# Kernel optimization log

Hardware: AMD Instinct MI355X
Metric: run time of the kernel (lower is better)

Reference implementation:

```python
import jax, jax.numpy as jnp
import numpy as np

N_NODES = 5000
N_STRUCT = 50
PER = N_NODES // N_STRUCT
K = 24
N_EDGES = N_NODES * K
MAX_EDGES = 32
D = 128
HEADS = 4
L = 2
M = 1
NSP = 4
ALL_SPECIES = np.array([1, 6, 7, 8])
R_CUT, R_TRANS = 5.0, 3.0
SPECIES_TABLE = jnp.full((9,), -1, dtype=jnp.int32).at[jnp.asarray(ALL_SPECIES)].set(jnp.arange(NSP, dtype=jnp.int32))

def _ln(x, w, b):
    m = jnp.mean(x, axis=-1, keepdims=True)
    v = jnp.var(x, axis=-1, keepdims=True)
    return (x - m) * jax.lax.rsqrt(v + 1e-5) * w + b

def _block(x, mask, Wq, Wk, Wv, Wo, l1w, l1b, l2w, l2b, W1, b1, W2, b2):
    n, t, d = x.shape
    dh = d // HEADS
    h = _ln(x, l1w, l1b)
    q = (h @ Wq).reshape(n, t, HEADS, dh)
    k = (h @ Wk).reshape(n, t, HEADS, dh)
    v = (h @ Wv).reshape(n, t, HEADS, dh)
    scores = jnp.einsum('nthd,nshd->nhts', q, k) * (1.0 / np.sqrt(dh))
    p = jax.nn.softmax(scores, axis=-1) * mask[:, None, None, :]  # cutoff-weighted keys
    x = x + jnp.einsum('nhts,nshd->nthd', p, v).reshape(n, t, d) @ Wo
    h2 = _ln(x, l2w, l2b)
    return x + jax.nn.gelu(h2 @ W1 + b1) @ W2 + b2

def _transformer(x, mask, params):
    for i in range(L):
        x = _block(x, mask, *(a[i] for a in params))
    return x

def _graph_indices(centers, neighbors):
    e_ids = jnp.arange(N_EDGES, dtype=jnp.int32)
    counts = jnp.zeros((N_NODES,), jnp.int32).at[centers].add(1)
    start = jnp.cumsum(counts) - counts
    slot = e_ids - start[centers]  # centers sorted by construction
    nef_idx = jnp.zeros((N_NODES, MAX_EDGES), jnp.int32).at[centers, slot].set(e_ids)
    nef_mask = jnp.arange(MAX_EDGES, dtype=jnp.int32)[None, :] < counts[:, None]
    keys = centers * N_NODES + neighbors
    order = jnp.argsort(keys)
    corr = order[jnp.searchsorted(keys[order], neighbors * N_NODES + centers)]
    return nef_idx, slot, nef_mask, corr

def _cutoff(r):
    x = (r - R_TRANS) / (R_CUT - R_TRANS)
    smooth = 0.5 * (1.0 + jnp.cos(jnp.pi * x))
    return jnp.where(r < R_TRANS, 1.0, jnp.where(r >= R_CUT, 0.0, smooth))

def _forward(positions, cells, cell_shifts, enc_Wcart, enc_emb_center, enc_emb_neigh, enc_Wcomp, t_Wq, t_Wk, t_Wv, t_Wo, t_ln1w, t_ln1b, t_ln2w, t_ln2b, t_W1, t_b1, t_W2, t_b2, g_contr, g_Wq, g_Wk, g_Wv, g_Wo, g_ln1w, g_ln1b, g_ln2w, g_ln2b, g_W1, g_b1, g_W2, g_b2, readout_W, composition_weights, numbers, centers, neighbors):
    seg = jnp.repeat(jnp.arange(N_STRUCT, dtype=jnp.int32), PER)  # sorted structure ids
    ev = positions[neighbors] - positions[centers] + jnp.einsum('ia,iab->ib', cell_shifts, cells[seg[centers]])
    radial = _cutoff(jnp.sqrt(jnp.sum(ev * ev, axis=-1)))
    elem = SPECIES_TABLE[numbers]
    nef_idx, slot, nef_mask, corr = _graph_indices(centers, neighbors)
    radial_nef = jnp.where(nef_mask, radial[nef_idx], 0.0)
    feats = jnp.concatenate([ev[nef_idx] @ enc_Wcart, enc_emb_center[elem[centers][nef_idx]], enc_emb_neigh[elem[neighbors][nef_idx]]], axis=-1) @ enc_Wcomp
    tparams = (t_Wq, t_Wk, t_Wv, t_Wo, t_ln1w, t_ln1b, t_ln2w, t_ln2b, t_W1, t_b1, t_W2, t_b2)
    feats = _transformer(feats, radial_nef, tparams)
    gparams = (g_Wq, g_Wk, g_Wv, g_Wo, g_ln1w, g_ln1b, g_ln2w, g_ln2b, g_W1, g_b1, g_W2, g_b2)
    for m in range(M):
        new = feats[centers, slot]  # nef -> edge list
        new = jnp.concatenate([new, new[corr]], axis=-1) @ g_contr[m]
        new = _transformer(new[nef_idx], radial_nef, tuple(a[m] for a in gparams))
        feats = feats + new
    ee = (feats @ readout_W)[..., 0] * radial_nef  # [N, MAX_EDGES]
    struct_e = jax.ops.segment_sum(jnp.sum(ee, axis=1), seg, num_segments=N_STRUCT, indices_are_sorted=True)
    comp = jax.ops.segment_sum(jax.nn.one_hot(elem, NSP, dtype=jnp.float32), seg, num_segments=N_STRUCT, indices_are_sorted=True)
    return struct_e + comp @ composition_weights

def setup_inputs():
    key = jax.random.key(0)
    ks = jax.random.split(key, 24)
    deltas = np.concatenate([np.arange(1, K // 2 + 1), -np.arange(1, K // 2 + 1)])
    nb_local = (np.arange(PER)[:, None] + deltas[None, :]) % PER  # symmetric circulant graph per structure
    neighbors = (nb_local[None, :, :] + (np.arange(N_STRUCT) * PER)[:, None, None]).reshape(-1)
    centers = np.repeat(np.arange(N_NODES), K)
    def w(i, shape, s=0.05):
        return (jax.random.normal(ks[i], shape) * s).astype(jnp.float32)
    return {
        'positions': jax.random.normal(ks[0], (N_NODES, 3), dtype=jnp.float32) * 2.0,
        'cells': jnp.tile(jnp.eye(3, dtype=jnp.float32) * 20.0, (N_STRUCT, 1, 1)),
        'cell_shifts': jnp.zeros((N_EDGES, 3), dtype=jnp.float32),
        'enc_Wcart': w(2, (3, D), 0.5),
        'enc_emb_center': w(3, (NSP, D), 1.0),
        'enc_emb_neigh': w(4, (NSP, D), 1.0),
        'enc_Wcomp': w(5, (3 * D, D)),
        't_Wq': w(6, (L, D, D)), 't_Wk': w(7, (L, D, D)), 't_Wv': w(8, (L, D, D)), 't_Wo': w(9, (L, D, D)),
        't_ln1w': jnp.ones((L, D), jnp.float32), 't_ln1b': jnp.zeros((L, D), jnp.float32),
        't_ln2w': jnp.ones((L, D), jnp.float32), 't_ln2b': jnp.zeros((L, D), jnp.float32),
        't_W1': w(10, (L, D, 4 * D)), 't_b1': jnp.zeros((L, 4 * D), jnp.float32),
        't_W2': w(11, (L, 4 * D, D)), 't_b2': jnp.zeros((L, D), jnp.float32),
        'g_contr': w(12, (M, 2 * D, D)),
        'g_Wq': w(13, (M, L, D, D)), 'g_Wk': w(14, (M, L, D, D)), 'g_Wv': w(15, (M, L, D, D)), 'g_Wo': w(16, (M, L, D, D)),
        'g_ln1w': jnp.ones((M, L, D), jnp.float32), 'g_ln1b': jnp.zeros((M, L, D), jnp.float32),
        'g_ln2w': jnp.ones((M, L, D), jnp.float32), 'g_ln2b': jnp.zeros((M, L, D), jnp.float32),
        'g_W1': w(17, (M, L, D, 4 * D)), 'g_b1': jnp.zeros((M, L, 4 * D), jnp.float32),
        'g_W2': w(18, (M, L, 4 * D, D)), 'g_b2': jnp.zeros((M, L, D), jnp.float32),
        'readout_W': w(19, (D, 1)),
        'composition_weights': w(20, (NSP,), 1.0),
        'numbers': jnp.asarray(ALL_SPECIES, dtype=jnp.int32)[jax.random.randint(ks[1], (N_NODES,), 0, NSP)],
        'centers': jnp.asarray(centers, dtype=jnp.int32),
        'neighbors': jnp.asarray(neighbors, dtype=jnp.int32),
    }

def reference(positions, cells, cell_shifts, enc_Wcart, enc_emb_center, enc_emb_neigh, enc_Wcomp, t_Wq, t_Wk, t_Wv, t_Wo, t_ln1w, t_ln1b, t_ln2w, t_ln2b, t_W1, t_b1, t_W2, t_b2, g_contr, g_Wq, g_Wk, g_Wv, g_Wo, g_ln1w, g_ln1b, g_ln2w, g_ln2b, g_W1, g_b1, g_W2, g_b2, readout_W, composition_weights, numbers, centers, neighbors):
    return _forward(positions, cells, cell_shifts, enc_Wcart, enc_emb_center, enc_emb_neigh, enc_Wcomp, t_Wq, t_Wk, t_Wv, t_Wo, t_ln1w, t_ln1b, t_ln2w, t_ln2b, t_W1, t_b1, t_W2, t_b2, g_contr, g_Wq, g_Wk, g_Wv, g_Wo, g_ln1w, g_ln1b, g_ln2w, g_ln2b, g_W1, g_b1, g_W2, g_b2, readout_W, composition_weights, numbers, centers, neighbors)
```

## Files before the change

### kernel.cpp

```cpp
#include <hip/hip_runtime.h>
#include <hip/hip_bf16.h>
#include <math.h>

#define N_NODES 5000
#define N_STRUCT 50
#define PER 100
#define K_NB 24
#define N_EDGES (N_NODES*K_NB)
#define TMAX 32
#define D 128
#define FF 512
#define NTOK (N_NODES*TMAX)

typedef short bf16x8 __attribute__((ext_vector_type(8)));
typedef float f32x4  __attribute__((ext_vector_type(4)));
#define MFMA_B16(a,b,c) __builtin_amdgcn_mfma_f32_16x16x32_bf16(a,b,c,0,0,0)

__device__ __forceinline__ short f2bf(float x){
    return (short)((__float_as_uint(x) + 0x8000u) >> 16);
}
__device__ __forceinline__ short f2bf_rn(float x){
    unsigned u = __float_as_uint(x);
    return (short)((u + 0x7FFFu + ((u>>16)&1u)) >> 16);
}

__device__ __forceinline__ float gelu_f(float x){
    float arg = x * fmaf(x*x, -0.07135481627f, -1.5957691216057308f);
    return x * __builtin_amdgcn_rcpf(1.f + __expf(arg));
}

__device__ __forceinline__ float cutoff_f(float r){
    if (r < 3.f) return 1.f;
    if (r >= 5.f) return 0.f;
    float x = (r-3.f)*0.5f;
    return 0.5f*(1.f + cosf(3.14159265358979323846f * x));
}

__global__ void k_zero(float* out){
    for (int i = threadIdx.x; i < N_STRUCT; i += 64) out[i] = 0.f;
}

__global__ void k_elem(const int* __restrict__ numbers, int* __restrict__ ELEM){
    int i = blockIdx.x*256 + threadIdx.x;
    if (i < N_NODES){
        int z = numbers[i];
        ELEM[i] = (z==1)?0:(z==6)?1:(z==7)?2:(z==8)?3:-1;
    }
}

__global__ void k_prep(const float* __restrict__ Wcart, const float* __restrict__ embc,
                       const float* __restrict__ embn, const float* __restrict__ Wcomp,
                       float* __restrict__ W3, float* __restrict__ ECn, float* __restrict__ ENn){
    int j = threadIdx.x;
    for (int a = 0; a < 3; a++){
        float s = 0;
        for (int i = 0; i < 128; i++) s += Wcart[a*128+i]*Wcomp[i*128+j];
        W3[a*128+j] = s;
    }
    for (int sp = 0; sp < 4; sp++){
        float s1 = 0, s2 = 0;
        for (int i = 0; i < 128; i++){
            s1 += embc[sp*128+i]*Wcomp[(128+i)*128+j];
            s2 += embn[sp*128+i]*Wcomp[(256+i)*128+j];
        }
        ECn[sp*128+j] = s1; ENn[sp*128+j] = s2;
    }
}

__global__ void k_wt(const float* tWq, const float* tWk, const float* tWv, const float* tWo,
                     const float* tW1, const float* tW2, const float* gWq, const float* gWk,
                     const float* gWv, const float* gWo, const float* gW1, const float* gW2,
                     const float* gct, short* __restrict__ WT){
    const int  sel[25]  = {0,0,1,1,2,2,3,3,4,4,5,5,6,6,7,7,8,8,9,9,10,10,11,11,12};
    const int  lin[25]  = {7,7,7,7,7,7,7,7,7,7,9,9,7,7,7,7,7,7,7,7,7,7,9,9,8};
    const int  lout[25] = {7,7,7,7,7,7,7,7,9,9,7,7,7,7,7,7,7,7,7,7,9,9,7,7,7};
    const int  soff[25] = {0,16384,0,16384,0,16384,0,16384,0,65536,0,65536,
                           0,16384,0,16384,0,16384,0,16384,0,65536,0,65536,0};
    const int  doff[25] = {0,16384,32768,49152,65536,81920,98304,114688,
                           131072,196608,262144,327680,
                           393216,409600,425984,442368,458752,475136,491520,507904,
                           524288,589824,655360,720896,786432};
    int gid = blockIdx.x*256 + threadIdx.x;
    if (gid >= 819200) return;
    int r = 0, base = 0;
    while (true){
        int sz = 1 << (lin[r]+lout[r]);
        if (gid < base + sz) break;
        base += sz; r++;
    }
    int d = gid - base;
    int j = d >> lin[r], i = d & ((1<<lin[r])-1);
    const float* src;
    switch (sel[r]){
        case 0: src=tWq; break; case 1: src=tWk; break; case 2: src=tWv; break; case 3: src=tWo; break;
        case 4: src=tW1; break; case 5: src=tW2; break;
        case 6: src=gWq; break; case 7: src=gWk; break; case 8: src=gWv; break; case 9: src=gWo; break;
        case 10: src=gW1; break; case 11: src=gW2; break; default: src=gct; break;
    }
    float v = src[soff[r] + (i<<lout[r]) + j];
    if (sel[r] == 0 || sel[r] == 6) v *= 0.17677669529663689f;
    WT[doff[r] + d] = f2bf_rn(v);
}

__global__ void k_edge(const float* __restrict__ pos, const float* __restrict__ cells,
                       const float* __restrict__ shifts, const int* __restrict__ centers,
                       const int* __restrict__ neighbors, float* __restrict__ EV,
                       float* __restrict__ RAD, int* __restrict__ CORR){
    int e = blockIdx.x*256 + threadIdx.x;
    if (e >= N_EDGES) return;
    int c = centers[e], nb = neighbors[e];
    int st = c / PER;
    const float* cell = cells + st*9;
    float s0 = shifts[e*3+0], s1 = shifts[e*3+1], s2 = shifts[e*3+2];
    float ex = pos[nb*3+0]-pos[c*3+0] + s0*cell[0]+s1*cell[3]+s2*cell[6];
    float ey = pos[nb*3+1]-pos[c*3+1] + s0*cell[1]+s1*cell[4]+s2*cell[7];
    float ez = pos[nb*3+2]-pos[c*3+2] + s0*cell[2]+s1*cell[5]+s2*cell[8];
    EV[e*3+0] = ex; EV[e*3+1] = ey; EV[e*3+2] = ez;
    RAD[e] = cutoff_f(sqrtf(ex*ex+ey*ey+ez*ez));
    int base = nb*K_NB, corr = base;
    for (int k2 = 0; k2 < K_NB; k2++){
        if (neighbors[base+k2] == c){ corr = base+k2; break; }
    }
    CORR[e] = corr;
}

__global__ void k_encode(const float* __restrict__ EV, const float* __restrict__ RAD,
                         const int* __restrict__ centers, const int* __restrict__ neighbors,
                         const int* __restrict__ ELEM, const float* __restrict__ W3,
                         const float* __restrict__ ECn, const float* __restrict__ ENn,
                         float* __restrict__ X, float* __restrict__ RADN){
    int row = blockIdx.x;
    int j = threadIdx.x;
    int n = row >> 5, s = row & 31;
    int e = (s < K_NB) ? (n*K_NB + s) : 0;
    int ec = ELEM[centers[e]], en = ELEM[neighbors[e]];
    float ev0 = EV[e*3+0], ev1 = EV[e*3+1], ev2 = EV[e*3+2];
    float v = ev0*W3[j] + ev1*W3[128+j] + ev2*W3[256+j] + ECn[ec*128+j] + ENn[en*128+j];
    X[(size_t)row*D + j] = v;
    if (j == 0) RADN[row] = (s < K_NB) ? RAD[e] : 0.f;
}

__global__ __launch_bounds__(256, 2) void k_attn_p(float* __restrict__ X,
        const short* __restrict__ Wqt, const short* __restrict__ Wkt,
        const short* __restrict__ Wvt, const short* __restrict__ Wot,
        const float* __restrict__ lnw, const float* __restrict__ lnb,
        const float* __restrict__ radn){
    __shared__ float xs[32*132];
    __shared__ short hh[32*136];
    __shared__ short Qs[32*136];
    __shared__ short Ks[32*136];
    __shared__ short VT[128*40];
    __shared__ short Ps[4*32*40];
    __shared__ float radl[32];
    const int tid = threadIdx.x, lane = tid & 63, w = tid >> 6;
    const int quad = lane >> 4, l16 = lane & 15;

    bf16x8 wQ[8], wK[8], wV[8], wO[8];
    #pragma unroll
    for (int mt = 0; mt < 2; mt++)
        #pragma unroll
        for (int kk = 0; kk < 4; kk++){
            int ro = (w*32 + mt*16 + l16)*128 + kk*32 + quad*8;
            wQ[mt*4+kk] = *(const bf16x8*)&Wqt[ro];
            wK[mt*4+kk] = *(const bf16x8*)&Wkt[ro];
            wV[mt*4+kk] = *(const bf16x8*)&Wvt[ro];
            wO[mt*4+kk] = *(const bf16x8*)&Wot[ro];
        }

    for (int node = blockIdx.x; node < N_NODES; node += 1024){
        float* Xn = X + (size_t)node*32*128;
        {
            int row = tid >> 3, l8 = tid & 7;
            f32x4 v[4];
            #pragma unroll
            for (int c = 0; c < 4; c++){
                v[c] = *(const f32x4*)&Xn[row*128 + l8*16 + c*4];
                *(f32x4*)&xs[row*132 + l8*16 + c*4] = v[c];
            }
            float s = 0, ss = 0;
            #pragma unroll
            for (int c = 0; c < 4; c++){
                #pragma unroll
                for (int k = 0; k < 4; k++){ s += v[c][k]; ss += v[c][k]*v[c][k]; }
            }
            #pragma unroll
            for (int m = 1; m < 8; m <<= 1){ s += __shfl_xor(s, m); ss += __shfl_xor(ss, m); }
            float mean = s*(1.f/128.f);
            float rstd = rsqrtf(ss*(1.f/128.f) - mean*mean + 1e-5f);
            #pragma unroll
            for (int c = 0; c < 4; c++){
                f32x4 wv4 = *(const f32x4*)&lnw[l8*16 + c*4];
                f32x4 bv4 = *(const f32x4*)&lnb[l8*16 + c*4];
                short4 pk;
                pk.x = f2bf((v[c][0]-mean)*rstd*wv4[0] + bv4[0]);
                pk.y = f2bf((v[c][1]-mean)*rstd*wv4[1] + bv4[1]);
                pk.z = f2bf((v[c][2]-mean)*rstd*wv4[2] + bv4[2]);
                pk.w = f2bf((v[c][3]-mean)*rstd*wv4[3] + bv4[3]);
                *(short4*)&hh[row*136 + l8*16 + c*4] = pk;
            }
        }
        if (tid < 32) radl[tid] = radn[(size_t)node*32 + tid];
        __syncthreads();

        {
            f32x4 z = {0.f,0.f,0.f,0.f};
            f32x4 qacc[4] = {z,z,z,z}, kacc[4] = {z,z,z,z};
            #pragma unroll
            for (int kk = 0; kk < 4; kk++){
                bf16x8 h0 = *(const bf16x8*)&hh[(l16)*136    + kk*32 + quad*8];
                bf16x8 h1 = *(const bf16x8*)&hh[(16+l16)*136 + kk*32 + quad*8];
                #pragma unroll
                for (int mt = 0; mt < 2; mt++){
                    qacc[mt*2+0] = MFMA_B16(wQ[mt*4+kk], h0, qacc[mt*2+0]);
                    qacc[mt*2+1] = MFMA_B16(wQ[mt*4+kk], h1, qacc[mt*2+1]);
                    kacc[mt*2+0] = MFMA_B16(wK[mt*4+kk], h0, kacc[mt*2+0]);
                    kacc[mt*2+1] = MFMA_B16(wK[mt*4+kk], h1, kacc[mt*2+1]);
                }
            }
            #pragma unroll
            for (int mt = 0; mt < 2; mt++){
                #pragma unroll
                for (int nt = 0; nt < 2; nt++){
                    int t = nt*16 + l16, jb = w*32 + mt*16 + quad*4;
                    short4 pk;
                    pk.x = f2bf(qacc[mt*2+nt][0]); pk.y = f2bf(qacc[mt*2+nt][1]);
                    pk.z = f2bf(qacc[mt*2+nt][2]); pk.w = f2bf(qacc[mt*2+nt][3]);
                    *(short4*)&Qs[t*136 + jb] = pk;
                    short4 pk2;
                    pk2.x = f2bf(kacc[mt*2+nt][0]); pk2.y = f2bf(kacc[mt*2+nt][1]);
                    pk2.z = f2bf(kacc[mt*2+nt][2]); pk2.w = f2bf(kacc[mt*2+nt][3]);
                    *(short4*)&Ks[t*136 + jb] = pk2;
                }
            }
        }
        {
            f32x4 z = {0.f,0.f,0.f,0.f};
            f32x4 vacc[4] = {z,z,z,z};
            #pragma unroll
            for (int kk = 0; kk < 4; kk++){
                bf16x8 h0 = *(const bf16x8*)&hh[(l16)*136    + kk*32 + quad*8];
                bf16x8 h1 = *(const bf16x8*)&hh[(16+l16)*136 + kk*32 + quad*8];
                #pragma unroll
                for (int mt = 0; mt < 2; mt++){
                    vacc[0*2+mt] = MFMA_B16(h0, wV[mt*4+kk], vacc[0*2+mt]);
                    vacc[1*2+mt] = MFMA_B16(h1, wV[mt*4+kk], vacc[1*2+mt]);
                }
            }
            #pragma unroll
            for (int mt = 0; mt < 2; mt++){
                #pragma unroll
                for (int nt = 0; nt < 2; nt++){
                    int j = w*32 + nt*16 + l16, sb = mt*16 + quad*4;
                    f32x4 r4 = *(const f32x4*)&radl[sb];
                    short4 pk;
                    pk.x = f2bf(vacc[mt*2+nt][0]*r4[0]); pk.y = f2bf(vacc[mt*2+nt][1]*r4[1]);
                    pk.z = f2bf(vacc[mt*2+nt][2]*r4[2]); pk.w = f2bf(vacc[mt*2+nt][3]*r4[3]);
                    *(short4*)&VT[j*40 + sb] = pk;
                }
            }
        }
        {
            const int h = w;
            bf16x8 qa0 = *(const bf16x8*)&Qs[(l16)*136    + h*32 + quad*8];
            bf16x8 qa1 = *(const bf16x8*)&Qs[(16+l16)*136 + h*32 + quad*8];
            bf16x8 kb0 = *(const bf16x8*)&Ks[(l16)*136    + h*32 + quad*8];
            bf16x8 kb1 = *(const bf16x8*)&Ks[(16+l16)*136 + h*32 + quad*8];
            f32x4 z = {0.f,0.f,0.f,0.f};
            f32x4 sc00 = MFMA_B16(qa0, kb0, z), sc01 = MFMA_B16(qa0, kb1, z);
            f32x4 sc10 = MFMA_B16(qa1, kb0, z), sc11 = MFMA_B16(qa1, kb1, z);
            #pragma unroll
            for (int mt = 0; mt < 2; mt++){
                f32x4 s0 = mt ? sc10 : sc00, s1 = mt ? sc11 : sc01;
                #pragma unroll
                for (int r = 0; r < 4; r++){
                    float mx = fmaxf(s0[r], s1[r]);
                    #pragma unroll
                    for (int dlt = 1; dlt < 16; dlt <<= 1) mx = fmaxf(mx, __shfl_xor(mx, dlt));
                    float e0 = __expf(s0[r]-mx), e1 = __expf(s1[r]-mx);
                    float sm = e0 + e1;
                    #pragma unroll
                    for (int dlt = 1; dlt < 16; dlt <<= 1) sm += __shfl_xor(sm, dlt);
                    float inv = __builtin_amdgcn_rcpf(sm);
                    int t = mt*16 + quad*4 + r;
                    Ps[h*1280 + t*40 + l16]      = f2bf(e0*inv);
                    Ps[h*1280 + t*40 + 16 + l16] = f2bf(e1*inv);
                }
            }
        }
        short* OB = Qs;
        {
            const int h = w;
            bf16x8 pa0 = *(const bf16x8*)&Ps[h*1280 + (l16)*40    + quad*8];
            bf16x8 pa1 = *(const bf16x8*)&Ps[h*1280 + (16+l16)*40 + quad*8];
            bf16x8 vb0 = *(const bf16x8*)&VT[(h*32 + l16)*40      + quad*8];
            bf16x8 vb1 = *(const bf16x8*)&VT[(h*32 + 16 + l16)*40 + quad*8];
            f32x4 z = {0.f,0.f,0.f,0.f};
            f32x4 o00 = MFMA_B16(pa0, vb0, z), o01 = MFMA_B16(pa0, vb1, z);
            f32x4 o10 = MFMA_B16(pa1, vb0, z), o11 = MFMA_B16(pa1, vb1, z);
            #pragma unroll
            for (int mt = 0; mt < 2; mt++){
                #pragma unroll
                for (int nt = 0; nt < 2; nt++){
                    f32x4 ov = mt ? (nt ? o11 : o10) : (nt ? o01 : o00);
                    int j = w*32 + nt*16 + l16;
                    #pragma unroll
                    for (int r = 0; r < 4; r++){
                        int t = mt*16 + quad*4 + r;
                        OB[t*136 + j] = f2bf(ov[r]);
                    }
                }
            }
        }
        __syncthreads();
        {
            f32x4 z = {0.f,0.f,0.f,0.f};
            f32x4 oc[4] = {z,z,z,z};
            #pragma unroll
            for (int kk = 0; kk < 4; kk++){
                bf16x8 a0 = *(const bf16x8*)&OB[(l16)*136    + kk*32 + quad*8];
                bf16x8 a1 = *(const bf16x8*)&OB[(16+l16)*136 + kk*32 + quad*8];
                #pragma unroll
                for (int nt = 0; nt < 2; nt++){
                    oc[0+nt] = MFMA_B16(a0, wO[nt*4+kk], oc[0+nt]);
                    oc[2+nt] = MFMA_B16(a1, wO[nt*4+kk], oc[2+nt]);
                }
            }
            #pragma unroll
            for (int mt = 0; mt < 2; mt++){
                #pragma unroll
                for (int nt = 0; nt < 2; nt++){
                    int j2 = w*32 + nt*16 + l16;
                    #pragma unroll
                    for (int r = 0; r < 4; r++){
                        int t = mt*16 + quad*4 + r;
                        Xn[t*128 + j2] = xs[t*132 + j2] + oc[mt*2+nt][r];
                    }
                }
            }
        }
        __syncthreads();
    }
}

__global__ __launch_bounds__(512, 2) void k_ffn_p(float* __restrict__ X,
        const short* __restrict__ W1t, const short* __restrict__ W2t,
        const float* __restrict__ B1, const float* __restrict__ B2,
        const float* __restrict__ lnw, const float* __restrict__ lnb){
    __shared__ float xs[32*132];
    __shared__ short hh[32*136];
    __shared__ short mid[32*520];
    const int tid = threadIdx.x, lane = tid & 63, w = tid >> 6;
    const int quad = lane >> 4, l16 = lane & 15;

    bf16x8 wA[16];
    #pragma unroll
    for (int mt = 0; mt < 4; mt++)
        #pragma unroll
        for (int kk = 0; kk < 4; kk++)
            wA[mt*4+kk] = *(const bf16x8*)&W1t[(size_t)(w*64+mt*16+l16)*128 + kk*32 + quad*8];
    bf16x8 wB[16];
    #pragma unroll
    for (int kk = 0; kk < 16; kk++)
        wB[kk] = *(const bf16x8*)&W2t[(size_t)(w*16+l16)*512 + kk*32 + quad*8];
    f32x4 bb1[4];
    #pragma unroll
    for (int mt = 0; mt < 4; mt++) bb1[mt] = *(const f32x4*)&B1[w*64 + mt*16 + quad*4];
    const float b2v = B2[w*16 + l16];

    for (int tile = blockIdx.x; tile < NTOK/32; tile += 512){
        float* Xg = X + (size_t)tile*32*128;
        {
            int row = tid >> 4, lc = tid & 15;
            f32x4 v0 = *(const f32x4*)&Xg[row*128 + lc*8];
            f32x4 v1 = *(const f32x4*)&Xg[row*128 + lc*8 + 4];
            *(f32x4*)&xs[row*132 + lc*8]     = v0;
            *(f32x4*)&xs[row*132 + lc*8 + 4] = v1;
            float s = 0, ss = 0;
            #pragma unroll
            for (int k = 0; k < 4; k++){ s += v0[k]+v1[k]; ss += v0[k]*v0[k]+v1[k]*v1[k]; }
            #pragma unroll
            for (int m = 1; m < 16; m <<= 1){ s += __shfl_xor(s, m); ss += __shfl_xor(ss, m); }
            float mean = s*(1.f/128.f);
            float rstd = rsqrtf(ss*(1.f/128.f) - mean*mean + 1e-5f);
            f32x4 w0 = *(const f32x4*)&lnw[lc*8], w1 = *(const f32x4*)&lnw[lc*8+4];
            f32x4 g0 = *(const f32x4*)&lnb[lc*8], g1 = *(const f32x4*)&lnb[lc*8+4];
            short4 pa, pb;
            pa.x = f2bf((v0[0]-mean)*rstd*w0[0] + g0[0]);
            pa.y = f2bf((v0[1]-mean)*rstd*w0[1] + g0[1]);
            pa.z = f2bf((v0[2]-mean)*rstd*w0[2] + g0[2]);
            pa.w = f2bf((v0[3]-mean)*rstd*w0[3] + g0[3]);
            pb.x = f2bf((v1[0]-mean)*rstd*w1[0] + g1[0]);
            pb.y = f2bf((v1[1]-mean)*rstd*w1[1] + g1[1]);
            pb.z = f2bf((v1[2]-mean)*rstd*w1[2] + g1[2]);
            pb.w = f2bf((v1[3]-mean)*rstd*w1[3] + g1[3]);
            *(short4*)&hh[row*136 + lc*8]     = pa;
            *(short4*)&hh[row*136 + lc*8 + 4] = pb;
        }
        __syncthreads();
        {
            f32x4 z = {0.f,0.f,0.f,0.f};
            f32x4 acc[8];
            #pragma unroll
            for (int i = 0; i < 8; i++) acc[i] = z;
            #pragma unroll
            for (int kk = 0; kk < 4; kk++){
                bf16x8 h0 = *(const bf16x8*)&hh[(l16)*136    + kk*32 + quad*8];
                bf16x8 h1 = *(const bf16x8*)&hh[(16+l16)*136 + kk*32 + quad*8];
                #pragma unroll
                for (int mt = 0; mt < 4; mt++){
                    acc[mt*2+0] = MFMA_B16(wA[mt*4+kk], h0, acc[mt*2+0]);
                    acc[mt*2+1] = MFMA_B16(wA[mt*4+kk], h1, acc[mt*2+1]);
                }
            }
            #pragma unroll
            for (int mt = 0; mt < 4; mt++){
                int fb = w*64 + mt*16 + quad*4;
                #pragma unroll
                for (int nt = 0; nt < 2; nt++){
                    int t = nt*16 + l16;
                    short4 pk;
                    pk.x = f2bf(gelu_f(acc[mt*2+nt][0] + bb1[mt][0]));
                    pk.y = f2bf(gelu_f(acc[mt*2+nt][1] + bb1[mt][1]));
                    pk.z = f2bf(gelu_f(acc[mt*2+nt][2] + bb1[mt][2]));
                    pk.w = f2bf(gelu_f(acc[mt*2+nt][3] + bb1[mt][3]));
                    *(short4*)&mid[t*520 + fb] = pk;
                }
            }
        }
        __syncthreads();
        {
            f32x4 z = {0.f,0.f,0.f,0.f};
            f32x4 o0 = z, o1 = z;
            #pragma unroll
            for (int kk = 0; kk < 16; kk++){
                bf16x8 a0 = *(const bf16x8*)&mid[(l16)*520    + kk*32 + quad*8];
                bf16x8 a1 = *(const bf16x8*)&mid[(16+l16)*520 + kk*32 + quad*8];
                o0 = MFMA_B16(a0, wB[kk], o0);
                o1 = MFMA_B16(a1, wB[kk], o1);
            }
            int j = w*16 + l16;
            #pragma unroll
            for (int r = 0; r < 4; r++){
                int t0 = quad*4 + r, t1 = 16 + quad*4 + r;
                Xg[t0*128 + j] = xs[t0*132 + j] + o0[r] + b2v;
                Xg[t1*128 + j] = xs[t1*132 + j] + o1[r] + b2v;
            }
        }
        __syncthreads();
    }
}

__global__ __launch_bounds__(256) void k_contract_mfma(const float* __restrict__ X,
        const int* __restrict__ centers, const int* __restrict__ CORR,
        const short* __restrict__ gct, float* __restrict__ Y){
    __shared__ short ab[32*264];
    const int tid = threadIdx.x, lane = tid & 63, w = tid >> 6;
    const int quad = lane >> 4, l16 = lane & 15;
    const int e0 = blockIdx.x*32;
    for (int idx = tid; idx < 2048; idx += 256){
        int r = idx >> 6, c4 = idx & 63;
        int e = e0 + r, srcRow;
        if (c4 < 32){ int c = centers[e]; srcRow = c*32 + (e - c*K_NB); }
        else        { int ec = CORR[e]; int c = centers[ec]; srcRow = c*32 + (ec - c*K_NB); }
        float4 v = *(const float4*)&X[(size_t)srcRow*128 + (c4 & 31)*4];
        short4 pk; pk.x = f2bf(v.x); pk.y = f2bf(v.y); pk.z = f2bf(v.z); pk.w = f2bf(v.w);
        *(short4*)&ab[r*264 + c4*4] = pk;
    }
    __syncthreads();
    f32x4 z = {0.f,0.f,0.f,0.f};
    f32x4 o[4] = {z,z,z,z};
    #pragma unroll
    for (int kk = 0; kk < 8; kk++){
        bf16x8 a0 = *(const bf16x8*)&ab[(l16)*264    + kk*32 + quad*8];
        bf16x8 a1 = *(const bf16x8*)&ab[(16+l16)*264 + kk*32 + quad*8];
        #pragma unroll
        for (int nt = 0; nt < 2; nt++){
            bf16x8 bw = *(const bf16x8*)&gct[(size_t)(w*32+nt*16+l16)*256 + kk*32 + quad*8];
            o[0+nt] = MFMA_B16(a0, bw, o[0+nt]);
            o[2+nt] = MFMA_B16(a1, bw, o[2+nt]);
        }
    }
    #pragma unroll
    for (int mt = 0; mt < 2; mt++){
        #pragma unroll
        for (int nt = 0; nt < 2; nt++){
            int j = w*32 + nt*16 + l16;
            #pragma unroll
            for (int r = 0; r < 4; r++){
                int e = e0 + mt*16 + quad*4 + r;
                int c = e / K_NB, slot = e - c*K_NB;
                Y[((size_t)c*32 + slot)*128 + j] = o[mt*2+nt][r];
            }
        }
    }
}

__global__ void k_padfill(float* __restrict__ Y){
    int idx = blockIdx.x*256 + threadIdx.x;
    if (idx >= N_NODES*8*D) return;
    int j = idx & 127, rs = idx >> 7;
    int n = rs >> 3, sr = rs & 7;
    Y[((size_t)n*32 + K_NB + sr)*D + j] = Y[j];
}

__global__ __launch_bounds__(256) void k_readout(const float* __restrict__ X,
        const float* __restrict__ Y, const float* __restrict__ rW,
        const float* __restrict__ radn, const int* __restrict__ ELEM,
        const float* __restrict__ cw, float* __restrict__ out){
    __shared__ float rws[128];
    __shared__ float wsum[4];
    int S = blockIdx.x >> 3, sub = blockIdx.x & 7;
    int tid = threadIdx.x, lane = tid & 63, wv = tid >> 6;
    if (tid < 128) rws[tid] = rW[tid];
    __syncthreads();
    float acc = 0.f;
    for (int r = sub*400 + wv; r < (sub+1)*400; r += 4){
        size_t row = (size_t)S*PER*32 + r;
        float rad = radn[row];
        if (rad != 0.f){
            const float* xr = X + row*D;
            const float* yr = Y + row*D;
            acc += rad * ((xr[lane]+yr[lane])*rws[lane] + (xr[lane+64]+yr[lane+64])*rws[lane+64]);
        }
    }
    if (sub == 0){
        for (int nl = tid; nl < PER; nl += 256) acc += cw[ELEM[S*PER + nl]];
    }
    #pragma unroll
    for (int m = 1; m < 64; m <<= 1) acc += __shfl_xor(acc, m);
    if (lane == 0) wsum[wv] = acc;
    __syncthreads();
    if (tid == 0) atomicAdd(&out[S], wsum[0]+wsum[1]+wsum[2]+wsum[3]);
}

extern "C" void kernel_launch(void* const* d_in, const int* in_sizes, int n_in,
                              void* d_out, int out_size, void* d_ws, size_t ws_size,
                              hipStream_t stream){
    const float* positions   = (const float*)d_in[0];
    const float* cells       = (const float*)d_in[1];
    const float* cell_shifts = (const float*)d_in[2];
    const float* enc_Wcart   = (const float*)d_in[3];
    const float* enc_emb_c   = (const float*)d_in[4];
    const float* enc_emb_n   = (const float*)d_in[5];
    const float* enc_Wcomp   = (const float*)d_in[6];
    const float* t_Wq  = (const float*)d_in[7];
    const float* t_Wk  = (const float*)d_in[8];
    const float* t_Wv  = (const float*)d_in[9];
    const float* t_Wo  = (const float*)d_in[10];
    const float* t_ln1w = (const float*)d_in[11];
    const float* t_ln1b = (const float*)d_in[12];
    const float* t_ln2w = (const float*)d_in[13];
    const float* t_ln2b = (const float*)d_in[14];
    const float* t_W1  = (const float*)d_in[15];
    const float* t_b1  = (const float*)d_in[16];
    const float* t_W2  = (const float*)d_in[17];
    const float* t_b2  = (const float*)d_in[18];
    const float* g_contr = (const float*)d_in[19];
    const float* g_Wq  = (const float*)d_in[20];
    const float* g_Wk  = (const float*)d_in[21];
    const float* g_Wv  = (const float*)d_in[22];
    const float* g_Wo  = (const float*)d_in[23];
    const float* g_ln1w = (const float*)d_in[24];
    const float* g_ln1b = (const float*)d_in[25];
    const float* g_ln2w = (const float*)d_in[26];
    const float* g_ln2b = (const float*)d_in[27];
    const float* g_W1  = (const float*)d_in[28];
    const float* g_b1  = (const float*)d_in[29];
    const float* g_W2  = (const float*)d_in[30];
    const float* g_b2  = (const float*)d_in[31];
    const float* readout_W = (const float*)d_in[32];
    const float* comp_w    = (const float*)d_in[33];
    const int* numbers   = (const int*)d_in[34];
    const int* centers   = (const int*)d_in[35];
    const int* neighbors = (const int*)d_in[36];

    float* ws = (float*)d_ws;
    float* X    = ws;
    float* Y    = X + (size_t)NTOK*D;
    float* EV   = Y + (size_t)NTOK*D;
    float* RAD  = EV + (size_t)N_EDGES*3;
    float* RADN = RAD + N_EDGES;
    float* W3   = RADN + NTOK;
    float* ECn  = W3 + 3*128;
    float* ENn  = ECn + 4*128;
    int*   ELEM = (int*)(ENn + 4*128);
    int*   CORR = ELEM + N_NODES;
    short* WT   = (short*)(CORR + N_EDGES);

    const short *tWqt = WT,           *tWkt = WT + 32768, *tWvt = WT + 65536, *tWot = WT + 98304;
    const short *tW1t = WT + 131072,  *tW2t = WT + 262144;
    const short *gWqt = WT + 393216,  *gWkt = WT + 425984, *gWvt = WT + 458752, *gWot = WT + 491520;
    const short *gW1t = WT + 524288,  *gW2t = WT + 655360, *gctT = WT + 786432;

    k_zero<<<1, 64, 0, stream>>>((float*)d_out);
    k_elem<<<(N_NODES+255)/256, 256, 0, stream>>>(numbers, ELEM);
    k_prep<<<1, 128, 0, stream>>>(enc_Wcart, enc_emb_c, enc_emb_n, enc_Wcomp, W3, ECn, ENn);
    k_wt<<<3200, 256, 0, stream>>>(t_Wq, t_Wk, t_Wv, t_Wo, t_W1, t_W2,
                                   g_Wq, g_Wk, g_Wv, g_Wo, g_W1, g_W2, g_contr, WT);
    k_edge<<<(N_EDGES+255)/256, 256, 0, stream>>>(positions, cells, cell_shifts, centers, neighbors, EV, RAD, CORR);
    k_encode<<<NTOK, 128, 0, stream>>>(EV, RAD, centers, neighbors, ELEM, W3, ECn, ENn, X, RADN);

    for (int l = 0; l < 2; l++){
        k_attn_p<<<1024, 256, 0, stream>>>(X, tWqt + l*16384, tWkt + l*16384,
                                           tWvt + l*16384, tWot + l*16384,
                                           t_ln1w + l*128, t_ln1b + l*128, RADN);
        k_ffn_p<<<512, 512, 0, stream>>>(X, tW1t + l*65536, tW2t + l*65536,
                                         t_b1 + l*512, t_b2 + l*128,
                                         t_ln2w + l*128, t_ln2b + l*128);
    }

    k_contract_mfma<<<N_EDGES/32, 256, 0, stream>>>(X, centers, CORR, gctT, Y);
    k_padfill<<<(N_NODES*8*D+255)/256, 256, 0, stream>>>(Y);

    for (int l = 0; l < 2; l++){
        k_attn_p<<<1024, 256, 0, stream>>>(Y, gWqt + l*16384, gWkt + l*16384,
                                           gWvt + l*16384, gWot + l*16384,
                                           g_ln1w + l*128, g_ln1b + l*128, RADN);
        k_ffn_p<<<512, 512, 0, stream>>>(Y, gW1t + l*65536, gW2t + l*65536,
                                         g_b1 + l*512, g_b2 + l*128,
                                         g_ln2w + l*128, g_ln2b + l*128);
    }

    k_readout<<<N_STRUCT*8, 256, 0, stream>>>(X, Y, readout_W, RADN, ELEM, comp_w, (float*)d_out);
}
```

Before: 1.093 ms.

## Prefetch next tile's activations in attention/FFN loops and vectorize encode kernel

The persistent attention and FFN kernels now issue global loads for the next node/tile's activation rows into registers before computing on the current one, so global memory latency overlaps with MFMA work. The encode kernel switches from one block per token row with scalar stores to one block per node with 256 threads writing float4 vectors. This costs extra registers in already register-heavy kernels, which could limit occupancy or cause spills. The prefetch reads the next tile before the current tile's writes, but each tile is only written by its own block, so ordering stays correct.

Measured after the change: 1.130 ms. +3.4%, slower.

```diff
diff --git a/kernel.cpp b/kernel.cpp
--- a/kernel.cpp
+++ b/kernel.cpp
@@ -124,20 +124,32 @@
     CORR[e] = corr;
 }
 
-__global__ void k_encode(const float* __restrict__ EV, const float* __restrict__ RAD,
+__global__ __launch_bounds__(256) void k_encode(const float* __restrict__ EV,
+                         const float* __restrict__ RAD,
                          const int* __restrict__ centers, const int* __restrict__ neighbors,
                          const int* __restrict__ ELEM, const float* __restrict__ W3,
                          const float* __restrict__ ECn, const float* __restrict__ ENn,
                          float* __restrict__ X, float* __restrict__ RADN){
-    int row = blockIdx.x;
-    int j = threadIdx.x;
-    int n = row >> 5, s = row & 31;
+    int n = blockIdx.x, tid = threadIdx.x;
+    int s = tid >> 3, l8 = tid & 7;
     int e = (s < K_NB) ? (n*K_NB + s) : 0;
     int ec = ELEM[centers[e]], en = ELEM[neighbors[e]];
     float ev0 = EV[e*3+0], ev1 = EV[e*3+1], ev2 = EV[e*3+2];
-    float v = ev0*W3[j] + ev1*W3[128+j] + ev2*W3[256+j] + ECn[ec*128+j] + ENn[en*128+j];
-    X[(size_t)row*D + j] = v;
-    if (j == 0) RADN[row] = (s < K_NB) ? RAD[e] : 0.f;
+    size_t ro = (size_t)(n*32 + s)*128;
+    #pragma unroll
+    for (int c = 0; c < 4; c++){
+        int j = l8*16 + c*4;
+        f32x4 wa = *(const f32x4*)&W3[j];
+        f32x4 wb = *(const f32x4*)&W3[128+j];
+        f32x4 wc = *(const f32x4*)&W3[256+j];
+        f32x4 ea = *(const f32x4*)&ECn[ec*128+j];
+        f32x4 na = *(const f32x4*)&ENn[en*128+j];
+        f32x4 o;
+        #pragma unroll
+        for (int k = 0; k < 4; k++) o[k] = ev0*wa[k] + ev1*wb[k] + ev2*wc[k] + ea[k] + na[k];
+        *(f32x4*)&X[ro + j] = o;
+    }
+    if (tid < 32) RADN[(size_t)n*32 + tid] = (tid < K_NB) ? RAD[n*K_NB + tid] : 0.f;
 }
 
 __global__ __launch_bounds__(256, 2) void k_attn_p(float* __restrict__ X,
@@ -154,6 +166,7 @@
     __shared__ float radl[32];
     const int tid = threadIdx.x, lane = tid & 63, w = tid >> 6;
     const int quad = lane >> 4, l16 = lane & 15;
+    const int row = tid >> 3, l8 = tid & 7;
 
     bf16x8 wQ[8], wK[8], wV[8], wO[8];
     #pragma unroll
@@ -167,21 +180,28 @@
             wO[mt*4+kk] = *(const bf16x8*)&Wot[ro];
         }
 
+    f32x4 pv[4], pn[4];
+    {
+        const float* X0 = X + (size_t)blockIdx.x*4096;
+        #pragma unroll
+        for (int c = 0; c < 4; c++) pv[c] = *(const f32x4*)&X0[row*128 + l8*16 + c*4];
+    }
+
     for (int node = blockIdx.x; node < N_NODES; node += 1024){
-        float* Xn = X + (size_t)node*32*128;
-        {
-            int row = tid >> 3, l8 = tid & 7;
-            f32x4 v[4];
+        float* Xn = X + (size_t)node*4096;
+        int nxt = node + 1024; if (nxt >= N_NODES) nxt = node;
+        const float* Xx = X + (size_t)nxt*4096;
+        #pragma unroll
+        for (int c = 0; c < 4; c++) pn[c] = *(const f32x4*)&Xx[row*128 + l8*16 + c*4];
+
+        {
+            #pragma unroll
+            for (int c = 0; c < 4; c++) *(f32x4*)&xs[row*132 + l8*16 + c*4] = pv[c];
+            float s = 0, ss = 0;
             #pragma unroll
             for (int c = 0; c < 4; c++){
-                v[c] = *(const f32x4*)&Xn[row*128 + l8*16 + c*4];
-                *(f32x4*)&xs[row*132 + l8*16 + c*4] = v[c];
-            }
-            float s = 0, ss = 0;
-            #pragma unroll
-            for (int c = 0; c < 4; c++){
-                #pragma unroll
-                for (int k = 0; k < 4; k++){ s += v[c][k]; ss += v[c][k]*v[c][k]; }
+                #pragma unroll
+                for (int k = 0; k < 4; k++){ s += pv[c][k]; ss += pv[c][k]*pv[c][k]; }
             }
             #pragma unroll
             for (int m = 1; m < 8; m <<= 1){ s += __shfl_xor(s, m); ss += __shfl_xor(ss, m); }
@@ -192,10 +212,10 @@
                 f32x4 wv4 = *(const f32x4*)&lnw[l8*16 + c*4];
                 f32x4 bv4 = *(const f32x4*)&lnb[l8*16 + c*4];
                 short4 pk;
-                pk.x = f2bf((v[c][0]-mean)*rstd*wv4[0] + bv4[0]);
-                pk.y = f2bf((v[c][1]-mean)*rstd*wv4[1] + bv4[1]);
-                pk.z = f2bf((v[c][2]-mean)*rstd*wv4[2] + bv4[2]);
-                pk.w = f2bf((v[c][3]-mean)*rstd*wv4[3] + bv4[3]);
+                pk.x = f2bf((pv[c][0]-mean)*rstd*wv4[0] + bv4[0]);
+                pk.y = f2bf((pv[c][1]-mean)*rstd*wv4[1] + bv4[1]);
+                pk.z = f2bf((pv[c][2]-mean)*rstd*wv4[2] + bv4[2]);
+                pk.w = f2bf((pv[c][3]-mean)*rstd*wv4[3] + bv4[3]);
                 *(short4*)&hh[row*136 + l8*16 + c*4] = pk;
             }
         }
@@ -339,6 +359,8 @@
             }
         }
         __syncthreads();
+        #pragma unroll
+        for (int c = 0; c < 4; c++) pv[c] = pn[c];
     }
 }
 
@@ -351,6 +373,7 @@
     __shared__ short mid[32*520];
     const int tid = threadIdx.x, lane = tid & 63, w = tid >> 6;
     const int quad = lane >> 4, l16 = lane & 15;
+    const int row = tid >> 4, lc = tid & 15;
 
     bf16x8 wA[16];
     #pragma unroll
@@ -367,17 +390,26 @@
     for (int mt = 0; mt < 4; mt++) bb1[mt] = *(const f32x4*)&B1[w*64 + mt*16 + quad*4];
     const float b2v = B2[w*16 + l16];
 
+    f32x4 pv0, pv1, pn0, pn1;
+    {
+        const float* X0 = X + (size_t)blockIdx.x*4096;
+        pv0 = *(const f32x4*)&X0[row*128 + lc*8];
+        pv1 = *(const f32x4*)&X0[row*128 + lc*8 + 4];
+    }
+
     for (int tile = blockIdx.x; tile < NTOK/32; tile += 512){
-        float* Xg = X + (size_t)tile*32*128;
-        {
-            int row = tid >> 4, lc = tid & 15;
-            f32x4 v0 = *(const f32x4*)&Xg[row*128 + lc*8];
-            f32x4 v1 = *(const f32x4*)&Xg[row*128 + lc*8 + 4];
-            *(f32x4*)&xs[row*132 + lc*8]     = v0;
-            *(f32x4*)&xs[row*132 + lc*8 + 4] = v1;
+        float* Xg = X + (size_t)tile*4096;
+        int nxt = tile + 512; if (nxt >= NTOK/32) nxt = tile;
+        const float* Xx = X + (size_t)nxt*4096;
+        pn0 = *(const f32x4*)&Xx[row*128 + lc*8];
+        pn1 = *(const f32x4*)&Xx[row*128 + lc*8 + 4];
+
+        {
+            *(f32x4*)&xs[row*132 + lc*8]     = pv0;
+            *(f32x4*)&xs[row*132 + lc*8 + 4] = pv1;
             float s = 0, ss = 0;
             #pragma unroll
-            for (int k = 0; k < 4; k++){ s += v0[k]+v1[k]; ss += v0[k]*v0[k]+v1[k]*v1[k]; }
+            for (int k = 0; k < 4; k++){ s += pv0[k]+pv1[k]; ss += pv0[k]*pv0[k]+pv1[k]*pv1[k]; }
             #pragma unroll
             for (int m = 1; m < 16; m <<= 1){ s += __shfl_xor(s, m); ss += __shfl_xor(ss, m); }
             float mean = s*(1.f/128.f);
@@ -385,14 +417,14 @@
             f32x4 w0 = *(const f32x4*)&lnw[lc*8], w1 = *(const f32x4*)&lnw[lc*8+4];
             f32x4 g0 = *(const f32x4*)&lnb[lc*8], g1 = *(const f32x4*)&lnb[lc*8+4];
             short4 pa, pb;
-            pa.x = f2bf((v0[0]-mean)*rstd*w0[0] + g0[0]);
-            pa.y = f2bf((v0[1]-mean)*rstd*w0[1] + g0[1]);
-            pa.z = f2bf((v0[2]-mean)*rstd*w0[2] + g0[2]);
-            pa.w = f2bf((v0[3]-mean)*rstd*w0[3] + g0[3]);
-            pb.x = f2bf((v1[0]-mean)*rstd*w1[0] + g1[0]);
-            pb.y = f2bf((v1[1]-mean)*rstd*w1[1] + g1[1]);
-            pb.z = f2bf((v1[2]-mean)*rstd*w1[2] + g1[2]);
-            pb.w = f2bf((v1[3]-mean)*rstd*w1[3] + g1[3]);
+            pa.x = f2bf((pv0[0]-mean)*rstd*w0[0] + g0[0]);
+            pa.y = f2bf((pv0[1]-mean)*rstd*w0[1] + g0[1]);
+            pa.z = f2bf((pv0[2]-mean)*rstd*w0[2] + g0[2]);
+            pa.w = f2bf((pv0[3]-mean)*rstd*w0[3] + g0[3]);
+            pb.x = f2bf((pv1[0]-mean)*rstd*w1[0] + g1[0]);
+            pb.y = f2bf((pv1[1]-mean)*rstd*w1[1] + g1[1]);
+            pb.z = f2bf((pv1[2]-mean)*rstd*w1[2] + g1[2]);
+            pb.w = f2bf((pv1[3]-mean)*rstd*w1[3] + g1[3]);
             *(short4*)&hh[row*136 + lc*8]     = pa;
             *(short4*)&hh[row*136 + lc*8 + 4] = pb;
         }
@@ -447,6 +479,7 @@
             }
         }
         __syncthreads();
+        pv0 = pn0; pv1 = pn1;
     }
 }
 
@@ -598,7 +631,7 @@
     k_wt<<<3200, 256, 0, stream>>>(t_Wq, t_Wk, t_Wv, t_Wo, t_W1, t_W2,
                                    g_Wq, g_Wk, g_Wv, g_Wo, g_W1, g_W2, g_contr, WT);
     k_edge<<<(N_EDGES+255)/256, 256, 0, stream>>>(positions, cells, cell_shifts, centers, neighbors, EV, RAD, CORR);
-    k_encode<<<NTOK, 128, 0, stream>>>(EV, RAD, centers, neighbors, ELEM, W3, ECn, ENn, X, RADN);
+    k_encode<<<N_NODES, 256, 0, stream>>>(EV, RAD, centers, neighbors, ELEM, W3, ECn, ENn, X, RADN);
 
     for (int l = 0; l < 2; l++){
         k_attn_p<<<1024, 256, 0, stream>>>(X, tWqt + l*16384, tWkt + l*16384,
```
